# Performance work log

Measured on AMD Instinct MI355X. Metric: run time of the kernel, lower is better.

## Reference

```python
import jax, jax.numpy as jnp
import numpy as np

B, N, DIM = 4, 2048, 128
HEADS, HEAD = 8, 128
INNER = HEADS * HEAD  # 1024
EPS = 1e-5


def setup_inputs() -> dict:
    key = jax.random.key(0)
    k0, k1, k2 = jax.random.split(key, 3)
    return {
        "x": jax.random.normal(k0, (B, N, DIM), jnp.float32),
        "ln_gamma": jnp.ones((DIM,), jnp.float32),
        "ln_beta": jnp.zeros((DIM,), jnp.float32),
        "w_qkv": jax.random.normal(k1, (3 * INNER, DIM), jnp.float32) * (DIM ** -0.5),
        "w_out": jax.random.normal(k2, (DIM, INNER), jnp.float32) * (INNER ** -0.5),
        "b_out": jnp.zeros((DIM,), jnp.float32),
    }


def _rope(t):
    """lucidrains-style rotary embedding over full last dim of t: [b,h,n,d]."""
    n, d = t.shape[-2], t.shape[-1]
    inv_freq = 1.0 / (10000.0 ** (jnp.arange(0, d, 2, dtype=jnp.float32) / d))
    freqs = jnp.arange(n, dtype=jnp.float32)[:, None] * inv_freq[None, :]  # [n, d/2]
    freqs = jnp.repeat(freqs, 2, axis=-1)  # interleaved duplicate -> [n, d]
    cos, sin = jnp.cos(freqs), jnp.sin(freqs)
    # rotate_half on interleaved pairs: (x1, x2) -> (-x2, x1)
    x1, x2 = t[..., 0::2], t[..., 1::2]
    rot = jnp.stack((-x2, x1), axis=-1).reshape(t.shape)
    return t * cos + rot * sin


def reference(x, ln_gamma, ln_beta, w_qkv, w_out, b_out):
    # LayerNorm
    mu = x.mean(-1, keepdims=True)
    var = x.var(-1, keepdims=True)
    xn = (x - mu) * jax.lax.rsqrt(var + EPS) * ln_gamma + ln_beta
    # QKV projection (bias-free)
    qkv = jnp.einsum('bnd,ed->bne', xn, w_qkv)  # [B, N, 3*INNER]
    q, k, v = jnp.split(qkv, 3, axis=-1)
    to_heads = lambda t: t.reshape(B, N, HEADS, HEAD).transpose(0, 2, 1, 3)
    q, k, v = to_heads(q), to_heads(k), to_heads(v)  # [B, H, N, HEAD]
    # Partial RoPE: rotate all but the last token; last token stays unrotated
    q = jnp.concatenate([_rope(q[:, :, :-1]), q[:, :, -1:]], axis=2)
    k = jnp.concatenate([_rope(k[:, :, :-1]), k[:, :, -1:]], axis=2)
    scale = HEAD ** -0.5
    dots = jnp.einsum('bhid,bhjd->bhij', q, k) * scale  # [B, H, N, N]
    attn = jax.nn.softmax(dots, axis=-1)
    out = jnp.einsum('bhij,bhjd->bhid', attn, v)
    out = out.transpose(0, 2, 1, 3).reshape(B, N, INNER)
    return out @ w_out.T + b_out
```

## Files before the change

### kernel.cpp

```cpp
#include <hip/hip_runtime.h>
#include <hip/hip_bf16.h>
#include <hip/hip_fp16.h>

#define B_      4
#define N_      2048
#define DIM_    128
#define HEADS_  8
#define HEAD_   128
#define INNER_  1024
#define QKV_    3072
#define EPS_    1e-5f
#define SCALE_  0.08838834764831845f
#define ROPE_C  0.20762050593046015f

typedef __attribute__((ext_vector_type(8))) short short8;
typedef __attribute__((ext_vector_type(4))) short short4v;
typedef __attribute__((ext_vector_type(4))) float f32x4;


__device__ __forceinline__ unsigned short f2bf(float f) {
    unsigned u = __builtin_bit_cast(unsigned, f);
    u = (u + 0x7fffu + ((u >> 16) & 1u)) >> 16;
    return (unsigned short)u;
}
__device__ __forceinline__ float bf2f(unsigned short h) {
    unsigned u = ((unsigned)h) << 16;
    return __builtin_bit_cast(float, u);
}
__device__ __forceinline__ unsigned pk2(float a, float b) {
    return (unsigned)f2bf(a) | ((unsigned)f2bf(b) << 16);
}
__device__ __forceinline__ short4v pack4(const float* e) {
    __hip_bfloat162 h0 = __float22bfloat162_rn(make_float2(e[0], e[1]));
    __hip_bfloat162 h1 = __float22bfloat162_rn(make_float2(e[2], e[3]));
    uint2 u;
    __builtin_memcpy(&u.x, &h0, 4);
    __builtin_memcpy(&u.y, &h1, 4);
    return __builtin_bit_cast(short4v, u);
}

__device__ __forceinline__ int kidx(int r, int chunk) {
    return r * 128 + ((chunk ^ (r & 7)) << 3);
}
__device__ __forceinline__ int vidx(int r, int chunk) {
    return r * 64 + ((chunk ^ (r & 7)) << 3);
}

__global__ __launch_bounds__(256) void k_ln(
    const float* __restrict__ x, const float* __restrict__ g,
    const float* __restrict__ be, unsigned short* __restrict__ xnb)
{
    const int w = threadIdx.x >> 6, l = threadIdx.x & 63;
    const int row = blockIdx.x * 4 + w;
    float2 v = *(const float2*)(x + (size_t)row * 128 + l * 2);
    float s = v.x + v.y, s2 = v.x * v.x + v.y * v.y;
#pragma unroll
    for (int off = 1; off < 64; off <<= 1) {
        s  += __shfl_xor(s, off);
        s2 += __shfl_xor(s2, off);
    }
    float mu = s * (1.f / 128.f);
    float var = s2 * (1.f / 128.f) - mu * mu;
    float rs = rsqrtf(var + EPS_);
    float2 gg = *(const float2*)(g + l * 2);
    float2 bb = *(const float2*)(be + l * 2);
    float ox = (v.x - mu) * rs * gg.x + bb.x;
    float oy = (v.y - mu) * rs * gg.y + bb.y;
    *(unsigned*)(xnb + (size_t)row * 128 + l * 2) = pk2(ox, oy);
}

__global__ __launch_bounds__(256) void k_cvt(
    const float* __restrict__ src, unsigned short* __restrict__ dst)
{
    size_t i = ((size_t)blockIdx.x * 256 + threadIdx.x) * 8;
    float4 f0 = *(const float4*)(src + i), f1 = *(const float4*)(src + i + 4);
    uint4 u = { pk2(f0.x, f0.y), pk2(f0.z, f0.w), pk2(f1.x, f1.y), pk2(f1.z, f1.w) };
    *(uint4*)(dst + i) = u;
}

__global__ __launch_bounds__(256) void k_qkvf(
    const unsigned short* __restrict__ xnb, const unsigned short* __restrict__ wb,
    unsigned short* __restrict__ Q, unsigned short* __restrict__ K,
    unsigned short* __restrict__ Vt)
{
    __shared__ unsigned short lA[128 * 136];
    __shared__ unsigned short lB[128 * 136];
    const int t = threadIdx.x;
    const int wv = t >> 6, l = t & 63;
    const int lm = l & 15, quad = l >> 4;
    const int row0 = blockIdx.x * 128;
    const int by   = blockIdx.y;
    const int e0   = by * 128;

#pragma unroll
    for (int i = 0; i < 8; ++i) {
        int c = t + 256 * i;  int r = c >> 4, c8 = c & 15;
        *(uint4*)&lA[r * 136 + c8 * 8] =
            *(const uint4*)(xnb + (size_t)(row0 + r) * 128 + c8 * 8);
        *(uint4*)&lB[r * 136 + c8 * 8] =
            *(const uint4*)(wb + (size_t)(e0 + r) * 128 + c8 * 8);
    }
    __syncthreads();

    short8 af[2][4];
#pragma unroll
    for (int mt = 0; mt < 2; ++mt)
#pragma unroll
        for (int ks = 0; ks < 4; ++ks)
            af[mt][ks] = *(short8*)&lA[(wv * 32 + mt * 16 + lm) * 136 + ks * 32 + quad * 8];

    f32x4 acc[2][8];
#pragma unroll
    for (int mt = 0; mt < 2; ++mt)
#pragma unroll
        for (int ct = 0; ct < 8; ++ct) acc[mt][ct] = (f32x4){0.f, 0.f, 0.f, 0.f};
#pragma unroll
    for (int ks = 0; ks < 4; ++ks) {
#pragma unroll
        for (int ct = 0; ct < 8; ++ct) {
            short8 b = *(short8*)&lB[(ct * 16 + lm) * 136 + ks * 32 + quad * 8];
            acc[0][ct] = __builtin_amdgcn_mfma_f32_16x16x32_bf16(af[0][ks], b, acc[0][ct], 0, 0, 0);
            acc[1][ct] = __builtin_amdgcn_mfma_f32_16x16x32_bf16(af[1][ks], b, acc[1][ct], 0, 0, 0);
        }
    }
    __syncthreads();

    const int b  = row0 >> 11;
    const int n0 = row0 & (N_ - 1);
    const int h  = by & 7;
    const int bh = b * 8 + h;

    if (by < 16) {
#pragma unroll
        for (int mt = 0; mt < 2; ++mt)
#pragma unroll
            for (int ct = 0; ct < 8; ++ct)
#pragma unroll
                for (int r = 0; r < 4; ++r)
                    lA[(wv * 32 + mt * 16 + quad * 4 + r) * 136 + ct * 16 + lm] =
                        f2bf(acc[mt][ct][r]);
        __syncthreads();

        const int r_loc = t >> 1, half = t & 1;
        const int n = n0 + r_loc;
        unsigned short* dst = (by < 8 ? Q : K) +
            ((size_t)bh * N_ + n) * HEAD_ + half * 64;
        const bool dorope = (n != N_ - 1);
#pragma unroll
        for (int j = 0; j < 8; ++j) {
            short8 vv = *(short8*)&lA[r_loc * 136 + half * 64 + j * 8];
            if (dorope) {
                unsigned short* pv = (unsigned short*)&vv;
#pragma unroll
                for (int p = 0; p < 4; ++p) {
                    int i0 = half * 32 + j * 4 + p;
                    float invf = exp2f(-(float)i0 * ROPE_C);
                    float th = (float)n * invf;
                    float cs = __cosf(th), sn = __sinf(th);
                    float e = bf2f(pv[2 * p]), o = bf2f(pv[2 * p + 1]);
                    pv[2 * p]     = f2bf(e * cs - o * sn);
                    pv[2 * p + 1] = f2bf(o * cs + e * sn);
                }
            }
            *(short8*)(dst + j * 8) = vv;
        }
    } else {
#pragma unroll
        for (int mt = 0; mt < 2; ++mt)
#pragma unroll
            for (int ct = 0; ct < 8; ++ct)
#pragma unroll
                for (int r = 0; r < 4; ++r)
                    lA[(ct * 16 + lm) * 136 + wv * 32 + quad * 8 + mt * 4 + r] =
                        f2bf(acc[mt][ct][r]);
        __syncthreads();

        const int d = t >> 1, half = t & 1;
        unsigned short* dst = Vt + ((size_t)bh * HEAD_ + d) * N_ + n0 + half * 64;
#pragma unroll
        for (int j = 0; j < 8; ++j)
            *(short8*)(dst + j * 8) = *(short8*)&lA[d * 136 + half * 64 + j * 8];
    }
}

__global__ __launch_bounds__(256) void k_attn(
    const unsigned short* __restrict__ Q, const unsigned short* __restrict__ K,
    const unsigned short* __restrict__ Vt, unsigned short* __restrict__ Ob)
{
    __shared__ unsigned short lK[64 * 128];
    __shared__ unsigned short lV[128 * 64];

    const int t = threadIdx.x;
    const int w = t >> 6, l = t & 63;
    const int lm = l & 15, quad = l >> 4;
    const int bid = blockIdx.x;
    const int bh = bid & 31;
    const int qt = bid >> 5;
    const int n0 = qt * 128;
    const unsigned short* Qb = Q  + (size_t)bh * N_ * HEAD_;
    const unsigned short* Kb = K  + (size_t)bh * N_ * HEAD_;
    const unsigned short* Vb = Vt + (size_t)bh * N_ * HEAD_;

    short8 aq[2][4];
#pragma unroll
    for (int tt = 0; tt < 2; ++tt) {
        const unsigned short* qp =
            Qb + ((size_t)(n0 + tt * 64 + w * 16 + lm)) * 128 + quad * 8;
#pragma unroll
        for (int ks = 0; ks < 4; ++ks)
            aq[tt][ks] = *(const short8*)(qp + ks * 32);
    }

    f32x4 Oa[2][8];
#pragma unroll
    for (int tt = 0; tt < 2; ++tt)
#pragma unroll
        for (int i = 0; i < 8; ++i) Oa[tt][i] = (f32x4){0.f, 0.f, 0.f, 0.f};
    float ps0 = 0.f, ps1 = 0.f;
    const float C1 = SCALE_ * 1.44269504f;
    const float C0 = -23.08312f;

    short8 kr[4], vr[4];
#pragma unroll
    for (int i = 0; i < 4; ++i) {
        int c = t + 256 * i;
        kr[i] = *(const short8*)(Kb + ((size_t)(c >> 4)) * 128 + (c & 15) * 8);
        vr[i] = *(const short8*)(Vb + (size_t)(c >> 3) * N_ + (c & 7) * 8);
    }

    for (int jt = 0; jt < 32; ++jt) {
        __syncthreads();
#pragma unroll
        for (int i = 0; i < 4; ++i) {
            int c = t + 256 * i;
            *(short8*)&lK[kidx(c >> 4, c & 15)] = kr[i];
            *(short8*)&lV[vidx(c >> 3, c & 7)]  = vr[i];
        }
        __syncthreads();
        if (jt < 31) {
#pragma unroll
            for (int i = 0; i < 4; ++i) {
                int c = t + 256 * i;
                kr[i] = *(const short8*)(Kb + ((size_t)((jt + 1) * 64 + (c >> 4))) * 128 + (c & 15) * 8);
                vr[i] = *(const short8*)(Vb + (size_t)(c >> 3) * N_ + (jt + 1) * 64 + (c & 7) * 8);
            }
        }

        short4v pf0[4], pf1[4];
#pragma unroll
        for (int nb = 0; nb < 4; ++nb) {
            f32x4 st0 = (f32x4){0.f, 0.f, 0.f, 0.f};
            f32x4 st1 = (f32x4){0.f, 0.f, 0.f, 0.f};
#pragma unroll
            for (int ks = 0; ks < 4; ++ks) {
                short8 kf = *(short8*)&lK[kidx(nb * 16 + lm, (ks << 2) + quad)];
                st0 = __builtin_amdgcn_mfma_f32_16x16x32_bf16(kf, aq[0][ks], st0, 0, 0, 0);
                st1 = __builtin_amdgcn_mfma_f32_16x16x32_bf16(kf, aq[1][ks], st1, 0, 0, 0);
            }
            float e0[4], e1[4];
#pragma unroll
            for (int r = 0; r < 4; ++r) {
                e0[r] = exp2f(st0[r] * C1 + C0);
                e1[r] = exp2f(st1[r] * C1 + C0);
                ps0 += e0[r];  ps1 += e1[r];
            }
            pf0[nb] = pack4(e0);
            pf1[nb] = pack4(e1);
        }

#pragma unroll
        for (int c2 = 0; c2 < 2; ++c2) {
            short8 ap0 = __builtin_shufflevector(pf0[2 * c2], pf0[2 * c2 + 1],
                                                 0, 1, 2, 3, 4, 5, 6, 7);
            short8 ap1 = __builtin_shufflevector(pf1[2 * c2], pf1[2 * c2 + 1],
                                                 0, 1, 2, 3, 4, 5, 6, 7);
#pragma unroll
            for (int nb8 = 0; nb8 < 8; ++nb8) {
                short8 bv = *(short8*)&lV[vidx(nb8 * 16 + lm, (c2 << 2) + quad)];
                Oa[0][nb8] = __builtin_amdgcn_mfma_f32_16x16x32_bf16(ap0, bv, Oa[0][nb8], 0, 0, 0);
                Oa[1][nb8] = __builtin_amdgcn_mfma_f32_16x16x32_bf16(ap1, bv, Oa[1][nb8], 0, 0, 0);
            }
        }
    }

    ps0 += __shfl_xor(ps0, 16);  ps0 += __shfl_xor(ps0, 32);
    ps1 += __shfl_xor(ps1, 16);  ps1 += __shfl_xor(ps1, 32);

    const int b = bh >> 3, h = bh & 7;
#pragma unroll
    for (int tt = 0; tt < 2; ++tt)
#pragma unroll
        for (int r = 0; r < 4; ++r) {
            float lsum = __shfl(tt == 0 ? ps0 : ps1, (l & 48) | (quad * 4 + r));
            float il = 1.f / lsum;
            int n = n0 + tt * 64 + w * 16 + quad * 4 + r;
            unsigned short* op = Ob + ((size_t)b * N_ + n) * INNER_ + h * HEAD_ + lm;
#pragma unroll
            for (int nb8 = 0; nb8 < 8; ++nb8)
                op[nb8 * 16] = f2bf(Oa[tt][nb8][r] * il);
        }
}

__global__ __launch_bounds__(256) void k_attn2(
    const unsigned short* __restrict__ Q, const unsigned short* __restrict__ K,
    const unsigned short* __restrict__ Vt, float* __restrict__ Opart,
    float* __restrict__ psb)
{
    __shared__ unsigned short lK[64 * 128];
    __shared__ unsigned short lV[128 * 64];

    const int t = threadIdx.x;
    const int w = t >> 6, l = t & 63;
    const int lm = l & 15, quad = l >> 4;
    const int bid = blockIdx.x;
    const int s   = bid >> 9;
    const int p   = bid & 511;
    const int bh  = bid & 31;
    const int qt  = (bid >> 5) & 15;
    const int n0  = qt * 128;
    const int jt0 = s * 16;
    const unsigned short* Qb = Q  + (size_t)bh * N_ * HEAD_;
    const unsigned short* Kb = K  + (size_t)bh * N_ * HEAD_;
    const unsigned short* Vb = Vt + (size_t)bh * N_ * HEAD_;

    short8 aq[2][4];
#pragma unroll
    for (int tt = 0; tt < 2; ++tt) {
        const unsigned short* qp =
            Qb + ((size_t)(n0 + tt * 64 + w * 16 + lm)) * 128 + quad * 8;
#pragma unroll
        for (int ks = 0; ks < 4; ++ks)
            aq[tt][ks] = *(const short8*)(qp + ks * 32);
    }

    f32x4 Oa[2][8];
#pragma unroll
    for (int tt = 0; tt < 2; ++tt)
#pragma unroll
        for (int i = 0; i < 8; ++i) Oa[tt][i] = (f32x4){0.f, 0.f, 0.f, 0.f};
    float ps0 = 0.f, ps1 = 0.f;
    const float C1 = SCALE_ * 1.44269504f;
    const float C0 = -23.08312f;

    short8 kr[4], vr[4];
#pragma unroll
    for (int i = 0; i < 4; ++i) {
        int c = t + 256 * i;
        kr[i] = *(const short8*)(Kb + ((size_t)(jt0 * 64 + (c >> 4))) * 128 + (c & 15) * 8);
        vr[i] = *(const short8*)(Vb + (size_t)(c >> 3) * N_ + jt0 * 64 + (c & 7) * 8);
    }

    for (int jt = 0; jt < 16; ++jt) {
        __syncthreads();
#pragma unroll
        for (int i = 0; i < 4; ++i) {
            int c = t + 256 * i;
            *(short8*)&lK[kidx(c >> 4, c & 15)] = kr[i];
            *(short8*)&lV[vidx(c >> 3, c & 7)]  = vr[i];
        }
        __syncthreads();
        if (jt < 15) {
#pragma unroll
            for (int i = 0; i < 4; ++i) {
                int c = t + 256 * i;
                kr[i] = *(const short8*)(Kb + ((size_t)((jt0 + jt + 1) * 64 + (c >> 4))) * 128 + (c & 15) * 8);
                vr[i] = *(const short8*)(Vb + (size_t)(c >> 3) * N_ + (jt0 + jt + 1) * 64 + (c & 7) * 8);
            }
        }

        short4v pf0[4], pf1[4];
#pragma unroll
        for (int nb = 0; nb < 4; ++nb) {
            f32x4 st0 = (f32x4){0.f, 0.f, 0.f, 0.f};
            f32x4 st1 = (f32x4){0.f, 0.f, 0.f, 0.f};
#pragma unroll
            for (int ks = 0; ks < 4; ++ks) {
                short8 kf = *(short8*)&lK[kidx(nb * 16 + lm, (ks << 2) + quad)];
                st0 = __builtin_amdgcn_mfma_f32_16x16x32_bf16(kf, aq[0][ks], st0, 0, 0, 0);
                st1 = __builtin_amdgcn_mfma_f32_16x16x32_bf16(kf, aq[1][ks], st1, 0, 0, 0);
            }
            float e0[4], e1[4];
#pragma unroll
            for (int r = 0; r < 4; ++r) {
                e0[r] = exp2f(st0[r] * C1 + C0);
                e1[r] = exp2f(st1[r] * C1 + C0);
                ps0 += e0[r];  ps1 += e1[r];
            }
            pf0[nb] = pack4(e0);
            pf1[nb] = pack4(e1);
        }

#pragma unroll
        for (int c2 = 0; c2 < 2; ++c2) {
            short8 ap0 = __builtin_shufflevector(pf0[2 * c2], pf0[2 * c2 + 1],
                                                 0, 1, 2, 3, 4, 5, 6, 7);
            short8 ap1 = __builtin_shufflevector(pf1[2 * c2], pf1[2 * c2 + 1],
                                                 0, 1, 2, 3, 4, 5, 6, 7);
#pragma unroll
            for (int nb8 = 0; nb8 < 8; ++nb8) {
                short8 bv = *(short8*)&lV[vidx(nb8 * 16 + lm, (c2 << 2) + quad)];
                Oa[0][nb8] = __builtin_amdgcn_mfma_f32_16x16x32_bf16(ap0, bv, Oa[0][nb8], 0, 0, 0);
                Oa[1][nb8] = __builtin_amdgcn_mfma_f32_16x16x32_bf16(ap1, bv, Oa[1][nb8], 0, 0, 0);
            }
        }
    }

    ps0 += __shfl_xor(ps0, 16);  ps0 += __shfl_xor(ps0, 32);
    ps1 += __shfl_xor(ps1, 16);  ps1 += __shfl_xor(ps1, 32);

    float* Op = Opart + ((size_t)(s * 512 + p)) * 16384;
    float* pp = psb   + ((size_t)(s * 512 + p)) * 128;
#pragma unroll
    for (int tt = 0; tt < 2; ++tt)
#pragma unroll
        for (int r = 0; r < 4; ++r) {
            float lsum = __shfl(tt == 0 ? ps0 : ps1, (l & 48) | (quad * 4 + r));
            int rowl = tt * 64 + w * 16 + quad * 4 + r;
            if (lm == 0) pp[rowl] = lsum;
#pragma unroll
            for (int nb8 = 0; nb8 < 8; ++nb8)
                Op[rowl * 128 + nb8 * 16 + lm] = Oa[tt][nb8][r];
        }
}

__global__ __launch_bounds__(256) void k_comb(
    const float* __restrict__ Opart, const float* __restrict__ psb,
    unsigned short* __restrict__ Ob)
{
    __shared__ float inv[128];
    const int p = blockIdx.x;
    const int t = threadIdx.x;
    const int bh = p & 31, qt = p >> 5;
    if (t < 128) {
        float d = psb[(size_t)p * 128 + t] + psb[(size_t)(512 + p) * 128 + t];
        inv[t] = 1.f / d;
    }
    __syncthreads();
    const float* O0 = Opart + (size_t)p * 16384;
    const float* O1 = Opart + (size_t)(512 + p) * 16384;
    const int b = bh >> 3, h = bh & 7;
#pragma unroll
    for (int i = 0; i < 16; ++i) {
        int flat = i * 256 + t;
        int row = flat >> 5, dq = (flat & 31) * 4;
        float4 a = *(const float4*)(O0 + row * 128 + dq);
        float4 c = *(const float4*)(O1 + row * 128 + dq);
        float iv = inv[row];
        float e[4] = { (a.x + c.x) * iv, (a.y + c.y) * iv,
                       (a.z + c.z) * iv, (a.w + c.w) * iv };
        short4v o = pack4(e);
        int n = qt * 128 + row;
        *(short4v*)(Ob + ((size_t)b * N_ + n) * INNER_ + h * HEAD_ + dq) = o;
    }
}

__global__ __launch_bounds__(256) void k_proj(
    const unsigned short* __restrict__ Ob, const unsigned short* __restrict__ wob,
    const float* __restrict__ bias, float* __restrict__ out)
{
    __shared__ unsigned short lA[64 * 136];
    __shared__ unsigned short lB[64 * 136];
    float* lCf = (float*)lA;
    const int t = threadIdx.x;
    const int wv = t >> 6, l = t & 63;
    const int lm = l & 15, quad = l >> 4;
    const int row0 = blockIdx.x * 64;
    const int e0   = blockIdx.y * 64;

    f32x4 acc[4];
#pragma unroll
    for (int ct = 0; ct < 4; ++ct) acc[ct] = (f32x4){0.f, 0.f, 0.f, 0.f};

    for (int kt = 0; kt < 8; ++kt) {
        __syncthreads();
#pragma unroll
        for (int i = 0; i < 4; ++i) {
            int c = t + 256 * i;  int r = c >> 4, c8 = c & 15;
            *(uint4*)&lA[r * 136 + c8 * 8] =
                *(const uint4*)(Ob + (size_t)(row0 + r) * 1024 + kt * 128 + c8 * 8);
            *(uint4*)&lB[r * 136 + c8 * 8] =
                *(const uint4*)(wob + (size_t)(e0 + r) * 1024 + kt * 128 + c8 * 8);
        }
        __syncthreads();
        short8 a_[4];
#pragma unroll
        for (int ks = 0; ks < 4; ++ks)
            a_[ks] = *(short8*)&lA[(wv * 16 + lm) * 136 + ks * 32 + quad * 8];
#pragma unroll
        for (int ks = 0; ks < 4; ++ks)
#pragma unroll
            for (int ct = 0; ct < 4; ++ct) {
                short8 b = *(short8*)&lB[(ct * 16 + lm) * 136 + ks * 32 + quad * 8];
                acc[ct] = __builtin_amdgcn_mfma_f32_16x16x32_bf16(a_[ks], b, acc[ct], 0, 0, 0);
            }
    }
    __syncthreads();
#pragma unroll
    for (int ct = 0; ct < 4; ++ct)
#pragma unroll
        for (int r = 0; r < 4; ++r)
            lCf[(wv * 16 + quad * 4 + r) * 68 + ct * 16 + lm] = acc[ct][r];
    __syncthreads();
#pragma unroll
    for (int i = 0; i < 4; ++i) {
        int c = t + 256 * i;  int r = c >> 4, c4 = c & 15;
        float4 v = *(float4*)&lCf[r * 68 + c4 * 4];
        float4 b4 = *(const float4*)(bias + e0 + c4 * 4);
        v.x += b4.x; v.y += b4.y; v.z += b4.z; v.w += b4.w;
        *(float4*)(out + (size_t)(row0 + r) * 128 + e0 + c4 * 4) = v;
    }
}

extern "C" void kernel_launch(void* const* d_in, const int* in_sizes, int n_in,
                              void* d_out, int out_size, void* d_ws, size_t ws_size,
                              hipStream_t stream) {
    const float* x      = (const float*)d_in[0];
    const float* gamma  = (const float*)d_in[1];
    const float* beta   = (const float*)d_in[2];
    const float* w_qkv  = (const float*)d_in[3];
    const float* w_out  = (const float*)d_in[4];
    const float* b_out  = (const float*)d_in[5];
    float* out = (float*)d_out;
    char* wsb = (char*)d_ws;
    unsigned short* Q    = (unsigned short*)(wsb);
    unsigned short* K    = (unsigned short*)(wsb + (16ull << 20));
    unsigned short* Vt   = (unsigned short*)(wsb + (32ull << 20));
    unsigned short* Ob   = (unsigned short*)(wsb + (48ull << 20));
    unsigned short* xnb  = (unsigned short*)(wsb + (96ull << 20));
    unsigned short* wqb  = (unsigned short*)(wsb + (98ull << 20));
    unsigned short* wob  = (unsigned short*)(wsb + (99ull << 20));

    k_ln       <<<dim3(2048),    256, 0, stream>>>(x, gamma, beta, xnb);
    k_cvt      <<<dim3(192),     256, 0, stream>>>(w_qkv, wqb);
    k_cvt      <<<dim3(64),      256, 0, stream>>>(w_out, wob);
    k_qkvf     <<<dim3(64, 24),  256, 0, stream>>>(xnb, wqb, Q, K, Vt);

    if (ws_size >= (165ull << 20)) {
        float* Opart = (float*)(wsb + (100ull << 20));
        float* psb   = (float*)(wsb + (164ull << 20));
        k_attn2 <<<dim3(1024), 256, 0, stream>>>(Q, K, Vt, Opart, psb);
        k_comb  <<<dim3(512),  256, 0, stream>>>(Opart, psb, Ob);
    } else {
        k_attn  <<<dim3(512),  256, 0, stream>>>(Q, K, Vt, Ob);
    }
    k_proj     <<<dim3(128, 2),  256, 0, stream>>>(Ob, wob, b_out, out);
}
```

Baseline: 208.1 us.

## Load K/V tiles directly into LDS with global_load_lds instead of register staging

Replaces the register-staged K/V prefetch (global load to registers, then store to swizzled LDS) with direct global-to-LDS 16-byte loads in both attention kernels. The swizzle is moved to the source addresses so each lane writes a contiguous LDS slot. This frees the VGPRs that held the prefetched tiles and removes the explicit LDS store instructions. In exchange it drops the software prefetch of the next tile: each load is now issued and awaited inside the same barrier window, so global latency is no longer overlapped with compute unless occupancy hides it.

```diff
diff --git a/kernel.cpp b/kernel.cpp
--- a/kernel.cpp
+++ b/kernel.cpp
@@ -46,6 +46,12 @@
     return r * 64 + ((chunk ^ (r & 7)) << 3);
 }
 
+__device__ __forceinline__ void gl16(const void* g, void* l) {
+    __builtin_amdgcn_global_load_lds(
+        (const __attribute__((address_space(1))) void*)g,
+        (__attribute__((address_space(3))) void*)l, 16, 0, 0);
+}
+
 __global__ __launch_bounds__(256) void k_ln(
     const float* __restrict__ x, const float* __restrict__ g,
     const float* __restrict__ be, unsigned short* __restrict__ xnb)
@@ -220,31 +226,23 @@
     const float C1 = SCALE_ * 1.44269504f;
     const float C0 = -23.08312f;
 
-    short8 kr[4], vr[4];
-#pragma unroll
-    for (int i = 0; i < 4; ++i) {
-        int c = t + 256 * i;
-        kr[i] = *(const short8*)(Kb + ((size_t)(c >> 4)) * 128 + (c & 15) * 8);
-        vr[i] = *(const short8*)(Vb + (size_t)(c >> 3) * N_ + (c & 7) * 8);
-    }
+    const int rKb = w * 4 + (l >> 4);
+    const int cK  = ((l & 15) ^ (rKb & 7));
+    const int dVb = w * 8 + (l >> 3);
+    const int cV  = ((l & 7) ^ (l >> 3));
+    const unsigned short* pK = Kb + (size_t)rKb * 128 + cK * 8;
+    const unsigned short* pV = Vb + (size_t)dVb * (size_t)N_ + cV * 8;
 
     for (int jt = 0; jt < 32; ++jt) {
         __syncthreads();
 #pragma unroll
         for (int i = 0; i < 4; ++i) {
-            int c = t + 256 * i;
-            *(short8*)&lK[kidx(c >> 4, c & 15)] = kr[i];
-            *(short8*)&lV[vidx(c >> 3, c & 7)]  = vr[i];
-        }
-        __syncthreads();
-        if (jt < 31) {
-#pragma unroll
-            for (int i = 0; i < 4; ++i) {
-                int c = t + 256 * i;
-                kr[i] = *(const short8*)(Kb + ((size_t)((jt + 1) * 64 + (c >> 4))) * 128 + (c & 15) * 8);
-                vr[i] = *(const short8*)(Vb + (size_t)(c >> 3) * N_ + (jt + 1) * 64 + (c & 7) * 8);
-            }
-        }
+            gl16(pK + (size_t)i * (16 * 128), &lK[(i * 4 + w) * 512]);
+            gl16(pV + (size_t)i * (32 * (size_t)N_), &lV[(i * 4 + w) * 512]);
+        }
+        __syncthreads();
+        pK += 64 * 128;
+        pV += 64;
 
         short4v pf0[4], pf1[4];
 #pragma unroll
@@ -342,31 +340,23 @@
     const float C1 = SCALE_ * 1.44269504f;
     const float C0 = -23.08312f;
 
-    short8 kr[4], vr[4];
-#pragma unroll
-    for (int i = 0; i < 4; ++i) {
-        int c = t + 256 * i;
-        kr[i] = *(const short8*)(Kb + ((size_t)(jt0 * 64 + (c >> 4))) * 128 + (c & 15) * 8);
-        vr[i] = *(const short8*)(Vb + (size_t)(c >> 3) * N_ + jt0 * 64 + (c & 7) * 8);
-    }
+    const int rKb = w * 4 + (l >> 4);
+    const int cK  = ((l & 15) ^ (rKb & 7));
+    const int dVb = w * 8 + (l >> 3);
+    const int cV  = ((l & 7) ^ (l >> 3));
+    const unsigned short* pK = Kb + (size_t)(jt0 * 64 + rKb) * 128 + cK * 8;
+    const unsigned short* pV = Vb + (size_t)dVb * (size_t)N_ + jt0 * 64 + cV * 8;
 
     for (int jt = 0; jt < 16; ++jt) {
         __syncthreads();
 #pragma unroll
         for (int i = 0; i < 4; ++i) {
-            int c = t + 256 * i;
-            *(short8*)&lK[kidx(c >> 4, c & 15)] = kr[i];
-            *(short8*)&lV[vidx(c >> 3, c & 7)]  = vr[i];
-        }
-        __syncthreads();
-        if (jt < 15) {
-#pragma unroll
-            for (int i = 0; i < 4; ++i) {
-                int c = t + 256 * i;
-                kr[i] = *(const short8*)(Kb + ((size_t)((jt0 + jt + 1) * 64 + (c >> 4))) * 128 + (c & 15) * 8);
-                vr[i] = *(const short8*)(Vb + (size_t)(c >> 3) * N_ + (jt0 + jt + 1) * 64 + (c & 7) * 8);
-            }
-        }
+            gl16(pK + (size_t)i * (16 * 128), &lK[(i * 4 + w) * 512]);
+            gl16(pV + (size_t)i * (32 * (size_t)N_), &lV[(i * 4 + w) * 512]);
+        }
+        __syncthreads();
+        pK += 64 * 128;
+        pV += 64;
 
         short4v pf0[4], pf1[4];
 #pragma unroll
```

New measurement: 219.4 us. 1.05x slower.
